# Kernel optimization log

Measured on AMD Instinct MI355X. Metric: run time of the kernel, lower is better.

Reference implementation:

```python
import jax, jax.numpy as jnp
import numpy as np

H = 16       # num_heads (groups for complex conv)
A = 32       # num frequency anchors
KSZ = 5      # complex conv kernel size
PAD = (KSZ - 1) // 2  # circular padding, matches ComplexConv1DLayer


def setup_inputs() -> dict:
    key = jax.random.key(0)
    ks = jax.random.split(key, 12)
    B, N, D = 4, 2048, 1024
    hid, ghid = 256, 256  # pooling MLP hidden, gate MLP hidden
    F = N // 2 + 1

    def rn(k, shp, s=0.02):
        return jax.random.normal(k, shp, jnp.float32) * s

    return {
        "x": jax.random.normal(ks[0], (B, N, D), jnp.float32),
        "Wv": rn(ks[1], (D, D)), "bv": jnp.zeros((D,), jnp.float32),
        "Wp1": rn(ks[2], (D, hid)), "bp1": jnp.zeros((hid,), jnp.float32),
        "Wp2": rn(ks[3], (hid, 1)), "bp2": jnp.zeros((1,), jnp.float32),
        "Wg1": rn(ks[4], (D, ghid)), "bg1": jnp.zeros((ghid,), jnp.float32),
        "Wg2": rn(ks[5], (ghid, 2 * H * A)), "bg2": jnp.zeros((2 * H * A,), jnp.float32),
        "mod_bias": jnp.zeros((F,), jnp.float32),
        "conv_kr": rn(ks[6], (KSZ,), 1.0 / np.sqrt(KSZ)),
        "conv_ki": rn(ks[7], (KSZ,), 1.0 / np.sqrt(KSZ)),
        "Wo": rn(ks[8], (D, D)), "bo": jnp.zeros((D,), jnp.float32),
    }


def reference(x, Wv, bv, Wp1, bp1, Wp2, bp2, Wg1, bg1, Wg2, bg2,
              mod_bias, conv_kr, conv_ki, Wo, bo):
    B, N, D = x.shape
    dh = D // H
    F = N // 2 + 1

    # value projection -> per-head sequences, rFFT over sequence axis
    v = (x @ Wv + bv).reshape(B, N, H, dh).transpose(0, 2, 1, 3)   # (B,H,N,dh)
    Vf = jnp.fft.rfft(v, axis=2)                                   # (B,H,F,dh) complex64

    # AttentionPoolingLayer: two-layer MLP scores -> softmax over seq -> weighted sum
    s = jax.nn.gelu(x @ Wp1 + bp1, approximate=False) @ Wp2 + bp2  # (B,N,1)
    w = jax.nn.softmax(s, axis=1)
    g = jnp.sum(x * w, axis=1)                                     # (B,D)

    # gate MLP -> complex anchors (B,H,A)
    a = (jax.nn.gelu(g @ Wg1 + bg1, approximate=False) @ Wg2 + bg2).reshape(B, H, A, 2)
    anch_r, anch_i = a[..., 0], a[..., 1]

    # ComplexInterpolationLayer: cubic interpolation of anchors to F bins
    gr = jax.image.resize(anch_r, (B, H, F), method="cubic")
    gi = jax.image.resize(anch_i, (B, H, F), method="cubic")
    gate = gr + 1j * gi                                            # (B,H,F)

    # ComplexModReLULayer: ReLU(|z|+b) * z / |z| with per-frequency bias
    mag = jnp.abs(gate)
    gate = gate * (jax.nn.relu(mag + mod_bias) / (mag + 1e-8))

    # ComplexConv1DLayer: circular-pad complex conv along frequency
    gp = jnp.concatenate([gate[..., -PAD:], gate, gate[..., :PAD]], axis=-1)
    ker = conv_kr.astype(jnp.complex64) + 1j * conv_ki.astype(jnp.complex64)
    gate = sum(ker[j] * gp[..., j:j + F] for j in range(KSZ))      # (B,H,F)

    # spectral gating + inverse FFT + output projection
    y = jnp.fft.irfft(Vf * gate[..., None], n=N, axis=2)           # (B,H,N,dh)
    y = y.transpose(0, 2, 1, 3).reshape(B, N, D)
    return y @ Wo + bo
```

## Files before the change

kernel.cpp:

```cpp
#include <hip/hip_runtime.h>
#include <math.h>

#define NSEQ 2048
#define DMOD 1024
#define NBATCH 4
#define NHEAD 16
#define NFREQ 1025

typedef unsigned short u16t;
typedef __attribute__((ext_vector_type(8))) short short8;
typedef __attribute__((ext_vector_type(4))) float f32x4;

__device__ __forceinline__ float gelu_exact(float x) {
  return 0.5f * x * (1.0f + erff(x * 0.70710678118654752440f));
}
__device__ __forceinline__ u16t bf16_rtn(float x) {
  unsigned u = __float_as_uint(x);
  return (u16t)((u + 0x7FFFu + ((u >> 16) & 1u)) >> 16);
}
__device__ __forceinline__ float bf16f(u16t h) {
  return __uint_as_float(((unsigned)h) << 16);
}
__device__ __forceinline__ void gload_lds16(const u16t* g, u16t* l) {
  __builtin_amdgcn_global_load_lds(
      (const __attribute__((address_space(1))) void*)g,
      (__attribute__((address_space(3))) void*)l, 16, 0, 0);
}

__global__ __launch_bounds__(256) void split_kernel(const float* __restrict__ in,
    u16t* __restrict__ hi, u16t* __restrict__ lo, int n8) {
  for (int i = blockIdx.x * blockDim.x + threadIdx.x; i < n8; i += gridDim.x * blockDim.x) {
    const float4* p = reinterpret_cast<const float4*>(in + (size_t)i * 8);
    float4 a = p[0], b = p[1];
    float vv[8] = {a.x, a.y, a.z, a.w, b.x, b.y, b.z, b.w};
    alignas(16) u16t th[8];
    alignas(16) u16t tl[8];
#pragma unroll
    for (int e = 0; e < 8; ++e) {
      u16t h = bf16_rtn(vv[e]);
      th[e] = h;
      tl[e] = bf16_rtn(vv[e] - bf16f(h));
    }
    *reinterpret_cast<uint4*>(hi + (size_t)i * 8) = *reinterpret_cast<const uint4*>(th);
    *reinterpret_cast<uint4*>(lo + (size_t)i * 8) = *reinterpret_cast<const uint4*>(tl);
  }
}

__global__ __launch_bounds__(256) void tsplit_kernel(const float* __restrict__ W,
    u16t* __restrict__ Th, u16t* __restrict__ Tl, int K, int N) {
  __shared__ float tile[32][33];
  int k0 = blockIdx.y * 32, n0 = blockIdx.x * 32;
  int r = threadIdx.x >> 5, c = threadIdx.x & 31;
#pragma unroll
  for (int i = 0; i < 4; ++i)
    tile[r + 8 * i][c] = W[(size_t)(k0 + r + 8 * i) * N + n0 + c];
  __syncthreads();
#pragma unroll
  for (int i = 0; i < 4; ++i) {
    int rr = r + 8 * i;
    float v = tile[c][rr];
    u16t h = bf16_rtn(v);
    Th[(size_t)(n0 + rr) * K + k0 + c] = h;
    Tl[(size_t)(n0 + rr) * K + k0 + c] = bf16_rtn(v - bf16f(h));
  }
}

__global__ __launch_bounds__(256) void tsplit2_kernel(
    const float* __restrict__ Wv, u16t* __restrict__ Tvh, u16t* __restrict__ Tvl,
    const float* __restrict__ Wp, u16t* __restrict__ Tph, u16t* __restrict__ Tpl) {
  __shared__ float tile[32][33];
  int bx = blockIdx.x;
  const float* W; u16t* Th; u16t* Tl; int N, n0;
  if (bx < 32) { W = Wv; Th = Tvh; Tl = Tvl; N = 1024; n0 = bx * 32; }
  else         { W = Wp; Th = Tph; Tl = Tpl; N = 256;  n0 = (bx - 32) * 32; }
  const int K = 1024;
  int k0 = blockIdx.y * 32;
  int r = threadIdx.x >> 5, c = threadIdx.x & 31;
#pragma unroll
  for (int i = 0; i < 4; ++i)
    tile[r + 8 * i][c] = W[(size_t)(k0 + r + 8 * i) * N + n0 + c];
  __syncthreads();
#pragma unroll
  for (int i = 0; i < 4; ++i) {
    int rr = r + 8 * i;
    float v = tile[c][rr];
    u16t h = bf16_rtn(v);
    Th[(size_t)(n0 + rr) * K + k0 + c] = h;
    Tl[(size_t)(n0 + rr) * K + k0 + c] = bf16_rtn(v - bf16f(h));
  }
}

__global__ __launch_bounds__(256) void gemm_fused_kernel(
    const u16t* __restrict__ Ah_g, const u16t* __restrict__ Al_g,
    const u16t* __restrict__ Bvh, const u16t* __restrict__ Bvl,
    const u16t* __restrict__ Bph, const u16t* __restrict__ Bpl,
    const float* __restrict__ bv, const float* __restrict__ bp1,
    const float* __restrict__ Wp2,
    float* __restrict__ vT, float* __restrict__ s_part) {
  __shared__ u16t Ahs[128 * 64], Als[128 * 64], Bhs[128 * 64], Bls[128 * 64];
  __shared__ u16t Php[32 * 64], Ppl[32 * 64];
  const int tid = threadIdx.x;
  const int lane = tid & 63, wave = tid >> 6;
  const int lr = lane & 15, lg = lane >> 4;
  const int wm0 = (wave >> 1) * 64, wn0 = (wave & 1) * 64;
  const int nwg = gridDim.x;
  const int L = (blockIdx.x & 7) * (nwg >> 3) + (blockIdx.x >> 3);
  const int m0 = (L >> 3) * 128;
  const int nblk = L & 7;
  const int n0 = nblk * 128;
  const int pc0 = nblk * 32;
  const int K = 1024;

  f32x4 acc[4][4];
#pragma unroll
  for (int i = 0; i < 4; ++i)
#pragma unroll
    for (int j = 0; j < 4; ++j) acc[i][j] = 0.0f;
  f32x4 accp[2][2];
#pragma unroll
  for (int i = 0; i < 2; ++i)
#pragma unroll
    for (int j = 0; j < 2; ++j) accp[i][j] = 0.0f;

  for (int k0 = 0; k0 < K; k0 += 64) {
#pragma unroll
    for (int q = 0; q < 4; ++q) {
      int cid = q * 256 + tid;
      int row = cid >> 3, grp = cid & 7;
      int koff = k0 + ((grp ^ (row & 7)) << 3);
      size_t ea = (size_t)(m0 + row) * K + koff;
      size_t eb = (size_t)(n0 + row) * K + koff;
      int lbase = q * 2048 + wave * 512;
      gload_lds16(Ah_g + ea, Ahs + lbase);
      gload_lds16(Al_g + ea, Als + lbase);
      gload_lds16(Bvh + eb, Bhs + lbase);
      gload_lds16(Bvl + eb, Bls + lbase);
    }
    {
      int row = tid >> 3, grp = tid & 7;
      int koff = k0 + ((grp ^ (row & 7)) << 3);
      size_t ep = (size_t)(pc0 + row) * K + koff;
      int lbase = wave * 512;
      gload_lds16(Bph + ep, Php + lbase);
      gload_lds16(Bpl + ep, Ppl + lbase);
    }
    __syncthreads();
#pragma unroll
    for (int kf = 0; kf < 2; ++kf) {
      short8 ah[4], al[4];
#pragma unroll
      for (int mi = 0; mi < 4; ++mi) {
        int r_ = wm0 + mi * 16 + lr;
        int g = (kf * 4 + lg) ^ (r_ & 7);
        ah[mi] = *reinterpret_cast<const short8*>(&Ahs[r_ * 64 + g * 8]);
        al[mi] = *reinterpret_cast<const short8*>(&Als[r_ * 64 + g * 8]);
      }
#pragma unroll
      for (int ni = 0; ni < 4; ++ni) {
        int r_ = wn0 + ni * 16 + lr;
        int g = (kf * 4 + lg) ^ (r_ & 7);
        short8 bh8 = *reinterpret_cast<const short8*>(&Bhs[r_ * 64 + g * 8]);
        short8 bl8 = *reinterpret_cast<const short8*>(&Bls[r_ * 64 + g * 8]);
#pragma unroll
        for (int mi = 0; mi < 4; ++mi) {
          acc[mi][ni] = __builtin_amdgcn_mfma_f32_16x16x32_bf16(ah[mi], bh8, acc[mi][ni], 0, 0, 0);
          acc[mi][ni] = __builtin_amdgcn_mfma_f32_16x16x32_bf16(ah[mi], bl8, acc[mi][ni], 0, 0, 0);
          acc[mi][ni] = __builtin_amdgcn_mfma_f32_16x16x32_bf16(al[mi], bh8, acc[mi][ni], 0, 0, 0);
        }
      }
      short8 pah[2], pal[2];
#pragma unroll
      for (int mi = 0; mi < 2; ++mi) {
        int r_ = wave * 32 + mi * 16 + lr;
        int g = (kf * 4 + lg) ^ (r_ & 7);
        pah[mi] = *reinterpret_cast<const short8*>(&Ahs[r_ * 64 + g * 8]);
        pal[mi] = *reinterpret_cast<const short8*>(&Als[r_ * 64 + g * 8]);
      }
#pragma unroll
      for (int ni = 0; ni < 2; ++ni) {
        int r_ = ni * 16 + lr;
        int g = (kf * 4 + lg) ^ (r_ & 7);
        short8 pbh = *reinterpret_cast<const short8*>(&Php[r_ * 64 + g * 8]);
        short8 pbl = *reinterpret_cast<const short8*>(&Ppl[r_ * 64 + g * 8]);
#pragma unroll
        for (int mi = 0; mi < 2; ++mi) {
          accp[mi][ni] = __builtin_amdgcn_mfma_f32_16x16x32_bf16(pah[mi], pbh, accp[mi][ni], 0, 0, 0);
          accp[mi][ni] = __builtin_amdgcn_mfma_f32_16x16x32_bf16(pah[mi], pbl, accp[mi][ni], 0, 0, 0);
          accp[mi][ni] = __builtin_amdgcn_mfma_f32_16x16x32_bf16(pal[mi], pbh, accp[mi][ni], 0, 0, 0);
        }
      }
    }
    __syncthreads();
  }
#pragma unroll
  for (int mi = 0; mi < 4; ++mi)
#pragma unroll
    for (int ni = 0; ni < 4; ++ni) {
      int col = n0 + wn0 + ni * 16 + lr;
      float bvv = bv[col];
      f32x4 a = acc[mi][ni];
      int mbase = m0 + wm0 + mi * 16 + lg * 4;
      int b = mbase >> 11, ss = mbase & 2047;
      float4 o4;
      o4.x = a[0] + bvv; o4.y = a[1] + bvv; o4.z = a[2] + bvv; o4.w = a[3] + bvv;
      *reinterpret_cast<float4*>(vT + (size_t)b * (DMOD * NSEQ) + (size_t)col * NSEQ + ss) = o4;
    }
  {
    float w2[2], bcol[2];
#pragma unroll
    for (int ni = 0; ni < 2; ++ni) {
      int col = pc0 + ni * 16 + lr;
      w2[ni] = Wp2[col];
      bcol[ni] = bp1[col];
    }
#pragma unroll
    for (int mi = 0; mi < 2; ++mi)
#pragma unroll
      for (int r = 0; r < 4; ++r) {
        float p = 0.f;
#pragma unroll
        for (int ni = 0; ni < 2; ++ni)
          p = fmaf(gelu_exact(accp[mi][ni][r] + bcol[ni]), w2[ni], p);
        p += __shfl_xor(p, 1);
        p += __shfl_xor(p, 2);
        p += __shfl_xor(p, 4);
        p += __shfl_xor(p, 8);
        if (lr == 0) {
          int row = m0 + wave * 32 + mi * 16 + lg * 4 + r;
          s_part[nblk * 8192 + row] = p;
        }
      }
  }
}

template<int NBLK>
__global__ __launch_bounds__(256) void mfma_gemm(
    const u16t* __restrict__ Ah_g, const u16t* __restrict__ Al_g,
    const u16t* __restrict__ Bh_g, const u16t* __restrict__ Bl_g,
    const float* __restrict__ bias,
    float* __restrict__ Cf,
    int N, int K) {
  __shared__ u16t Ahs[128 * 64], Als[128 * 64], Bhs[128 * 64], Bls[128 * 64];
  const int tid = threadIdx.x;
  const int lane = tid & 63, wave = tid >> 6;
  const int lr = lane & 15, lg = lane >> 4;
  const int wm0 = (wave >> 1) * 64, wn0 = (wave & 1) * 64;
  const int nwg = gridDim.x;
  const int L = (blockIdx.x & 7) * (nwg >> 3) + (blockIdx.x >> 3);
  const int m0 = (L / NBLK) * 128, n0 = (L % NBLK) * 128;

  f32x4 acc[4][4];
#pragma unroll
  for (int i = 0; i < 4; ++i)
#pragma unroll
    for (int j = 0; j < 4; ++j) acc[i][j] = 0.0f;

  for (int k0 = 0; k0 < K; k0 += 64) {
#pragma unroll
    for (int q = 0; q < 4; ++q) {
      int cid = q * 256 + tid;
      int row = cid >> 3, grp = cid & 7;
      int koff = k0 + ((grp ^ (row & 7)) << 3);
      size_t ea = (size_t)(m0 + row) * K + koff;
      size_t eb = (size_t)(n0 + row) * K + koff;
      int lbase = q * 2048 + wave * 512;
      gload_lds16(Ah_g + ea, Ahs + lbase);
      gload_lds16(Al_g + ea, Als + lbase);
      gload_lds16(Bh_g + eb, Bhs + lbase);
      gload_lds16(Bl_g + eb, Bls + lbase);
    }
    __syncthreads();
#pragma unroll
    for (int kf = 0; kf < 2; ++kf) {
      short8 ah[4], al[4];
#pragma unroll
      for (int mi = 0; mi < 4; ++mi) {
        int r_ = wm0 + mi * 16 + lr;
        int g = (kf * 4 + lg) ^ (r_ & 7);
        ah[mi] = *reinterpret_cast<const short8*>(&Ahs[r_ * 64 + g * 8]);
        al[mi] = *reinterpret_cast<const short8*>(&Als[r_ * 64 + g * 8]);
      }
#pragma unroll
      for (int ni = 0; ni < 4; ++ni) {
        int r_ = wn0 + ni * 16 + lr;
        int g = (kf * 4 + lg) ^ (r_ & 7);
        short8 bh8 = *reinterpret_cast<const short8*>(&Bhs[r_ * 64 + g * 8]);
        short8 bl8 = *reinterpret_cast<const short8*>(&Bls[r_ * 64 + g * 8]);
#pragma unroll
        for (int mi = 0; mi < 4; ++mi) {
          acc[mi][ni] = __builtin_amdgcn_mfma_f32_16x16x32_bf16(ah[mi], bh8, acc[mi][ni], 0, 0, 0);
          acc[mi][ni] = __builtin_amdgcn_mfma_f32_16x16x32_bf16(ah[mi], bl8, acc[mi][ni], 0, 0, 0);
          acc[mi][ni] = __builtin_amdgcn_mfma_f32_16x16x32_bf16(al[mi], bh8, acc[mi][ni], 0, 0, 0);
        }
      }
    }
    __syncthreads();
  }
#pragma unroll
  for (int mi = 0; mi < 4; ++mi)
#pragma unroll
    for (int ni = 0; ni < 4; ++ni) {
      int col = n0 + wn0 + ni * 16 + lr;
      float bvv = bias[col];
      f32x4 a = acc[mi][ni];
#pragma unroll
      for (int r = 0; r < 4; ++r) {
        int row = m0 + wm0 + mi * 16 + lg * 4 + r;
        Cf[(size_t)row * N + col] = a[r] + bvv;
      }
    }
}

#define PADI(i) ((i) + ((i) >> 5))

template<int HJ, int TWS>
__device__ __forceinline__ void fwd_reg_stage(float* vr, float* vi,
    const float* TWr, const float* TWi, int lane) {
  float twr_[HJ], twi_[HJ];
#pragma unroll
  for (int t = 0; t < HJ; ++t) {
    int m = (t * 64 + lane) * TWS;
    twr_[t] = TWr[PADI(m)]; twi_[t] = TWi[PADI(m)];
  }
#pragma unroll
  for (int j = 0; j < 16; ++j) {
    if (j & HJ) continue;
    int t = j & (HJ - 1);
    float ur = vr[j], ui = vi[j];
    float wr = vr[j + HJ], wi = vi[j + HJ];
    float dr = ur - wr, di = ui - wi;
    vr[j] = ur + wr; vi[j] = ui + wi;
    vr[j + HJ] = dr * twr_[t] - di * twi_[t];
    vi[j + HJ] = dr * twi_[t] + di * twr_[t];
  }
}

template<int S, int TWS>
__device__ __forceinline__ void fwd_lane_stage(float* vr, float* vi,
    const float* TWr, const float* TWi, int lane) {
  float twr_ = 1.0f, twi_ = 0.0f;
  if (S > 1) {
    int m = (lane & (S - 1)) * TWS;
    twr_ = TWr[PADI(m)]; twi_ = TWi[PADI(m)];
  }
  bool hi = (lane & S) != 0;
#pragma unroll
  for (int j = 0; j < 16; ++j) {
    float or_ = __shfl_xor(vr[j], S, 64);
    float oi_ = __shfl_xor(vi[j], S, 64);
    float sr = vr[j] + or_, si_ = vi[j] + oi_;
    float dr = or_ - vr[j], di = oi_ - vi[j];
    float rr = dr * twr_ - di * twi_;
    float ri = dr * twi_ + di * twr_;
    vr[j] = hi ? rr : sr;
    vi[j] = hi ? ri : si_;
  }
}

template<int S, int TWS>
__device__ __forceinline__ void inv_lane_stage(float* vr, float* vi,
    const float* TWr, const float* TWi, int lane) {
  float twr_ = 1.0f, twi_ = 0.0f;
  if (S > 1) {
    int m = (lane & (S - 1)) * TWS;
    twr_ = TWr[PADI(m)]; twi_ = -TWi[PADI(m)];
  }
  bool hi = (lane & S) != 0;
#pragma unroll
  for (int j = 0; j < 16; ++j) {
    float xr = vr[j], xi = vi[j];
    if (S > 1) {
      float pr = xr * twr_ - xi * twi_;
      float pi = xr * twi_ + xi * twr_;
      xr = hi ? pr : xr;
      xi = hi ? pi : xi;
    }
    float or_ = __shfl_xor(xr, S, 64);
    float oi_ = __shfl_xor(xi, S, 64);
    vr[j] = hi ? (or_ - xr) : (xr + or_);
    vi[j] = hi ? (oi_ - xi) : (xi + oi_);
  }
}

template<int HJ, int TWS>
__device__ __forceinline__ void inv_reg_stage(float* vr, float* vi,
    const float* TWr, const float* TWi, int lane) {
  float twr_[HJ], twi_[HJ];
#pragma unroll
  for (int t = 0; t < HJ; ++t) {
    int m = (t * 64 + lane) * TWS;
    twr_[t] = TWr[PADI(m)]; twi_[t] = -TWi[PADI(m)];
  }
#pragma unroll
  for (int j = 0; j < 16; ++j) {
    if (j & HJ) continue;
    int t = j & (HJ - 1);
    float ur = vr[j], ui = vi[j];
    float br = vr[j + HJ], bi = vi[j + HJ];
    float wr = br * twr_[t] - bi * twi_[t];
    float wi = br * twi_[t] + bi * twr_[t];
    vr[j] = ur + wr; vi[j] = ui + wi;
    vr[j + HJ] = ur - wr; vi[j + HJ] = ui - wi;
  }
}

__global__ __launch_bounds__(256) void conv_fft_kernel(
    float* __restrict__ vio, const float* __restrict__ gateb) {
  __shared__ float Zr[4][1056], Zi[4][1056];
  __shared__ float TWr[528], TWi[528];
  const int tid = threadIdx.x;
  const int lane = tid & 63, wave = tid >> 6;
  const int c0 = blockIdx.x * 4;
  const int b = blockIdx.y;
  const int bh = b * NHEAD + (c0 >> 6);
  const float* gate_bh = gateb + (size_t)bh * NFREQ * 2;

#pragma unroll
  for (int q = 0; q < 2; ++q) {
    int m = q * 256 + tid;
    float si, co;
    sincosf(-3.14159265358979323846f * (float)m * (1.0f / 512.0f), &si, &co);
    TWr[PADI(m)] = co; TWi[PADI(m)] = si;
  }
  __syncthreads();

  float* zr = Zr[wave];
  float* zi = Zi[wave];
  float* col = vio + ((size_t)b * DMOD + (c0 + wave)) * NSEQ;

  float vr[16], vi[16];
#pragma unroll
  for (int j = 0; j < 16; ++j) {
    float2 w2 = *reinterpret_cast<const float2*>(col + 2 * (j * 64 + lane));
    vr[j] = w2.x; vi[j] = w2.y;
  }

  fwd_reg_stage<8, 1>(vr, vi, TWr, TWi, lane);
  fwd_reg_stage<4, 2>(vr, vi, TWr, TWi, lane);
  fwd_reg_stage<2, 4>(vr, vi, TWr, TWi, lane);
  fwd_reg_stage<1, 8>(vr, vi, TWr, TWi, lane);
  fwd_lane_stage<32, 16>(vr, vi, TWr, TWi, lane);
  fwd_lane_stage<16, 32>(vr, vi, TWr, TWi, lane);
  fwd_lane_stage<8, 64>(vr, vi, TWr, TWi, lane);
  fwd_lane_stage<4, 128>(vr, vi, TWr, TWi, lane);
  fwd_lane_stage<2, 256>(vr, vi, TWr, TWi, lane);
  fwd_lane_stage<1, 0>(vr, vi, TWr, TWi, lane);

#pragma unroll
  for (int j = 0; j < 16; ++j) {
    int p = PADI(j * 64 + lane);
    zr[p] = vr[j]; zi[p] = vi[j];
  }
  asm volatile("s_waitcnt lgkmcnt(0)" ::: "memory");

  const float s1 = 1.0f / 1024.0f;
#pragma unroll
  for (int q = 0; q < 8; ++q) {
    int k = q * 64 + lane;
    if (k == 0) {
      float z0r = zr[0], z0i = zi[0];
      float X0 = z0r + z0i;
      float XN = z0r - z0i;
      float2 G0 = *reinterpret_cast<const float2*>(gate_bh + 0);
      float2 GN = *reinterpret_cast<const float2*>(gate_bh + 1024 * 2);
      float y0 = X0 * G0.x * s1;
      float yN = XN * GN.x * s1;
      zr[0] = 0.5f * (y0 + yN); zi[0] = 0.5f * (y0 - yN);
      float zmr = zr[1], zmi = zi[1];
      float X5r = zmr, X5i = -zmi;
      float2 G5 = *reinterpret_cast<const float2*>(gate_bh + 512 * 2);
      float Y5r = (X5r * G5.x - X5i * G5.y) * s1;
      float Y5i = (X5r * G5.y + X5i * G5.x) * s1;
      zr[1] = Y5r; zi[1] = -Y5i;
    } else {
      int kq = 1024 - k;
      int rp = PADI((int)(__brev((unsigned)k) >> 22));
      int rq = PADI((int)(__brev((unsigned)kq) >> 22));
      float Zkr = zr[rp], Zki = zi[rp];
      float Zqr = zr[rq], Zqi = zi[rq];
      float Er = 0.5f * (Zkr + Zqr), Ei = 0.5f * (Zki - Zqi);
      float Odr = 0.5f * (Zki + Zqi), Odi = -0.5f * (Zkr - Zqr);
      float ti, tr;
      sincosf(-3.14159265358979323846f * (float)k * (1.0f / 1024.0f), &ti, &tr);
      float Pr = Odr * tr - Odi * ti, Pi = Odr * ti + Odi * tr;
      float Xkr = Er + Pr, Xki = Ei + Pi;
      float Xqr = Er - Pr, Xqi = -(Ei - Pi);
      float2 Gk = *reinterpret_cast<const float2*>(gate_bh + k * 2);
      float2 Gq = *reinterpret_cast<const float2*>(gate_bh + kq * 2);
      float Ykr = (Xkr * Gk.x - Xki * Gk.y) * s1;
      float Yki = (Xkr * Gk.y + Xki * Gk.x) * s1;
      float Yqr = (Xqr * Gq.x - Xqi * Gq.y) * s1;
      float Yqi = (Xqr * Gq.y + Xqi * Gq.x) * s1;
      float E2r = 0.5f * (Ykr + Yqr), E2i = 0.5f * (Yki - Yqi);
      float D2r = 0.5f * (Ykr - Yqr), D2i = 0.5f * (Yki + Yqi);
      float O2r = D2r * tr + D2i * ti, O2i = D2i * tr - D2r * ti;
      zr[rp] = E2r - O2i; zi[rp] = E2i + O2r;
      zr[rq] = E2r + O2i; zi[rq] = O2r - E2i;
    }
  }
  asm volatile("s_waitcnt lgkmcnt(0)" ::: "memory");

#pragma unroll
  for (int j = 0; j < 16; ++j) {
    int p = PADI(j * 64 + lane);
    vr[j] = zr[p]; vi[j] = zi[p];
  }
  asm volatile("s_waitcnt lgkmcnt(0)" ::: "memory");

  inv_lane_stage<1, 0>(vr, vi, TWr, TWi, lane);
  inv_lane_stage<2, 256>(vr, vi, TWr, TWi, lane);
  inv_lane_stage<4, 128>(vr, vi, TWr, TWi, lane);
  inv_lane_stage<8, 64>(vr, vi, TWr, TWi, lane);
  inv_lane_stage<16, 32>(vr, vi, TWr, TWi, lane);
  inv_lane_stage<32, 16>(vr, vi, TWr, TWi, lane);
  inv_reg_stage<1, 8>(vr, vi, TWr, TWi, lane);
  inv_reg_stage<2, 4>(vr, vi, TWr, TWi, lane);
  inv_reg_stage<4, 2>(vr, vi, TWr, TWi, lane);
  inv_reg_stage<8, 1>(vr, vi, TWr, TWi, lane);

#pragma unroll
  for (int j = 0; j < 16; ++j) {
    *reinterpret_cast<float2*>(col + 2 * (j * 64 + lane)) = make_float2(vr[j], vi[j]);
  }
}

__global__ __launch_bounds__(256) void tysplit_kernel(
    const float* __restrict__ yT, u16t* __restrict__ yh, u16t* __restrict__ yl) {
  __shared__ float tile[64][65];
  int t0 = blockIdx.x * 64, c0 = blockIdx.y * 64, b = blockIdx.z;
  int r = threadIdx.x >> 4;
  int cc = (threadIdx.x & 15) * 4;
#pragma unroll
  for (int i = 0; i < 4; ++i) {
    int row = r + 16 * i;
    float4 w = *reinterpret_cast<const float4*>(
        yT + ((size_t)b * DMOD + c0 + row) * NSEQ + t0 + cc);
    tile[row][cc] = w.x; tile[row][cc + 1] = w.y;
    tile[row][cc + 2] = w.z; tile[row][cc + 3] = w.w;
  }
  __syncthreads();
#pragma unroll
  for (int i = 0; i < 4; ++i) {
    int tt = r + 16 * i;
    alignas(8) u16t hh[4], ll[4];
#pragma unroll
    for (int e = 0; e < 4; ++e) {
      float v = tile[cc + e][tt];
      u16t h = bf16_rtn(v);
      hh[e] = h;
      ll[e] = bf16_rtn(v - bf16f(h));
    }
    size_t o = ((size_t)b * NSEQ + t0 + tt) * DMOD + c0 + cc;
    *reinterpret_cast<ushort4*>(yh + o) = *reinterpret_cast<const ushort4*>(hh);
    *reinterpret_cast<ushort4*>(yl + o) = *reinterpret_cast<const ushort4*>(ll);
  }
}

__global__ __launch_bounds__(256) void pool_partial_kernel(
    const float* __restrict__ x, const float* __restrict__ s_part,
    const float* __restrict__ bp2, float* __restrict__ gpart) {
  int chunk = blockIdx.x, b = blockIdx.y;
  int tid = threadIdx.x;
  __shared__ float red[256];
  __shared__ float wsh[128];
  float bp = bp2[0];
  float sv[8];
  float m = -1e30f;
#pragma unroll
  for (int q = 0; q < 8; ++q) {
    int row = b * NSEQ + q * 256 + tid;
    float v = bp;
#pragma unroll
    for (int c = 0; c < 8; ++c) v += s_part[c * 8192 + row];
    sv[q] = v;
    m = fmaxf(m, v);
  }
  red[tid] = m; __syncthreads();
  for (int o = 128; o; o >>= 1) { if (tid < o) red[tid] = fmaxf(red[tid], red[tid + o]); __syncthreads(); }
  float bm = red[0]; __syncthreads();
  float sum = 0.f;
#pragma unroll
  for (int q = 0; q < 8; ++q) sum += expf(sv[q] - bm);
  red[tid] = sum; __syncthreads();
  for (int o = 128; o; o >>= 1) { if (tid < o) red[tid] += red[tid + o]; __syncthreads(); }
  float inv = 1.0f / red[0];
  __syncthreads();
  int n0 = chunk * 128;
  if (tid < 128) {
    int row = b * NSEQ + n0 + tid;
    float v = bp;
#pragma unroll
    for (int c = 0; c < 8; ++c) v += s_part[c * 8192 + row];
    wsh[tid] = expf(v - bm) * inv;
  }
  __syncthreads();
  float acc[4] = {};
  for (int n = 0; n < 128; ++n) {
    float wn = wsh[n];
    const float* xr = &x[((size_t)b * NSEQ + n0 + n) * DMOD];
#pragma unroll
    for (int q = 0; q < 4; ++q) acc[q] = fmaf(wn, xr[tid + 256 * q], acc[q]);
  }
  float* gp = &gpart[((size_t)b * 16 + chunk) * DMOD];
#pragma unroll
  for (int q = 0; q < 4; ++q) gp[tid + 256 * q] = acc[q];
}

__global__ __launch_bounds__(256) void pool_reduce_mlp1_kernel(
    const float* __restrict__ gpart, const float* __restrict__ Wg1,
    float* __restrict__ part1) {
  int kb = blockIdx.x, b = blockIdx.y;
  int tid = threadIdx.x;
  int k0 = kb * 64;
  __shared__ float g_s[64];
  if (tid < 64) {
    float acc = 0.f;
#pragma unroll
    for (int j = 0; j < 16; ++j)
      acc += gpart[((size_t)b * 16 + j) * DMOD + k0 + tid];
    g_s[tid] = acc;
  }
  __syncthreads();
  float acc = 0.f;
#pragma unroll 8
  for (int i = 0; i < 64; ++i)
    acc = fmaf(g_s[i], Wg1[(size_t)(k0 + i) * 256 + tid], acc);
  part1[((size_t)b * 16 + kb) * 256 + tid] = acc;
}

__device__ __forceinline__ float keys_cubic(float x) {
  if (x >= 2.0f) return 0.0f;
  if (x >= 1.0f) return ((-0.5f * x + 2.5f) * x - 4.0f) * x + 2.0f;
  return ((1.5f * x - 2.5f) * x) * x + 1.0f;
}

__global__ __launch_bounds__(256) void gate_kernel(
    const float* __restrict__ part1, const float* __restrict__ bg1,
    const float* __restrict__ Wg2, const float* __restrict__ bg2,
    const float* __restrict__ mod_bias,
    const float* __restrict__ kr5, const float* __restrict__ ki5,
    float* __restrict__ gate_out) {
  int bh = blockIdx.x;
  int tid = threadIdx.x;
  __shared__ float hs_s[256];
  __shared__ float anch_s[64];
  __shared__ float ar_[32], ai_[32];
  __shared__ float gr[NFREQ], gi[NFREQ];
  int b = bh >> 4, h = bh & 15;
  {
    float a1 = bg1[tid];
#pragma unroll
    for (int j = 0; j < 16; ++j)
      a1 += part1[((size_t)b * 16 + j) * 256 + tid];
    hs_s[tid] = gelu_exact(a1);
  }
  __syncthreads();
  if (tid < 64) {
    int cc = h * 64 + tid;
    float a2 = bg2[cc];
    for (int i = 0; i < 256; ++i) a2 = fmaf(hs_s[i], Wg2[(size_t)i * 1024 + cc], a2);
    anch_s[tid] = a2;
  }
  __syncthreads();
  if (tid < 32) {
    ar_[tid] = anch_s[tid * 2 + 0];
    ai_[tid] = anch_s[tid * 2 + 1];
  }
  __syncthreads();
  const float inv_scale = 32.0f / 1025.0f;
  for (int f = tid; f < NFREQ; f += 256) {
    float c = (f + 0.5f) * inv_scale - 0.5f;
    int j0 = (int)floorf(c) - 1;
    float wr = 0.f, wi = 0.f, wsum = 0.f;
#pragma unroll
    for (int u = 0; u < 4; ++u) {
      int j = j0 + u;
      if (j < 0 || j > 31) continue;
      float w = keys_cubic(fabsf(c - (float)j));
      wsum += w;
      wr = fmaf(w, ar_[j], wr);
      wi = fmaf(w, ai_[j], wi);
    }
    float invw = 1.0f / wsum;
    wr *= invw; wi *= invw;
    float mag = sqrtf(wr * wr + wi * wi);
    float scale = fmaxf(mag + mod_bias[f], 0.0f) / (mag + 1e-8f);
    gr[f] = wr * scale;
    gi[f] = wi * scale;
  }
  __syncthreads();
  float k_r[5], k_i[5];
#pragma unroll
  for (int j = 0; j < 5; ++j) { k_r[j] = kr5[j]; k_i[j] = ki5[j]; }
  for (int f = tid; f < NFREQ; f += 256) {
    float cr = 0.f, ci = 0.f;
#pragma unroll
    for (int j = 0; j < 5; ++j) {
      int idx = f + j - 2;
      if (idx < 0) idx += NFREQ;
      else if (idx >= NFREQ) idx -= NFREQ;
      float a = gr[idx], bb = gi[idx];
      cr = fmaf(k_r[j], a, cr); cr = fmaf(-k_i[j], bb, cr);
      ci = fmaf(k_r[j], bb, ci); ci = fmaf(k_i[j], a, ci);
    }
    gate_out[((size_t)bh * NFREQ + f) * 2 + 0] = cr;
    gate_out[((size_t)bh * NFREQ + f) * 2 + 1] = ci;
  }
}

extern "C" void kernel_launch(void* const* d_in, const int* in_sizes, int n_in,
                              void* d_out, int out_size, void* d_ws, size_t ws_size,
                              hipStream_t stream) {
  const float* x        = (const float*)d_in[0];
  const float* Wv       = (const float*)d_in[1];
  const float* bv       = (const float*)d_in[2];
  const float* Wp1      = (const float*)d_in[3];
  const float* bp1      = (const float*)d_in[4];
  const float* Wp2      = (const float*)d_in[5];
  const float* bp2      = (const float*)d_in[6];
  const float* Wg1      = (const float*)d_in[7];
  const float* bg1      = (const float*)d_in[8];
  const float* Wg2      = (const float*)d_in[9];
  const float* bg2      = (const float*)d_in[10];
  const float* mod_bias = (const float*)d_in[11];
  const float* ckr      = (const float*)d_in[12];
  const float* cki      = (const float*)d_in[13];
  const float* Wo       = (const float*)d_in[14];
  const float* bo       = (const float*)d_in[15];

  const int M = NBATCH * NSEQ;
  const size_t MD = (size_t)M * DMOD;
  char* wsb = (char*)d_ws;

  u16t* x_hi = (u16t*)wsb;
  u16t* x_lo = x_hi + MD;
  u16t* y_hi = x_hi;
  u16t* y_lo = x_lo;
  u16t* WT_h = (u16t*)(wsb + (size_t)32 * 1024 * 1024);
  u16t* WT_l = (u16t*)(wsb + (size_t)34 * 1024 * 1024);
  u16t* WTp1_h = (u16t*)(wsb + (size_t)36 * 1024 * 1024);
  u16t* WTp1_l = (u16t*)(wsb + (size_t)36 * 1024 * 1024 + 524288);
  float* s_part = (float*)(wsb + (size_t)37 * 1024 * 1024);
  float* gpart = (float*)(wsb + (size_t)36 * 1024 * 1024);
  float* part1 = gpart + 65536;
  float* gateb = part1 + 4096;

  float* vT  = (float*)d_out;
  float* out = (float*)d_out;

  dim3 blk(256);

  split_kernel<<<dim3(2048), blk, 0, stream>>>(x, x_hi, x_lo, (int)(MD / 8));
  tsplit2_kernel<<<dim3(40, 32), blk, 0, stream>>>(Wv, WT_h, WT_l, Wp1, WTp1_h, WTp1_l);
  gemm_fused_kernel<<<dim3(512), blk, 0, stream>>>(
      x_hi, x_lo, WT_h, WT_l, WTp1_h, WTp1_l, bv, bp1, Wp2, vT, s_part);
  tsplit_kernel<<<dim3(1024 / 32, 1024 / 32), blk, 0, stream>>>(Wo, WT_h, WT_l, 1024, 1024);
  pool_partial_kernel<<<dim3(16, NBATCH), blk, 0, stream>>>(x, s_part, bp2, gpart);
  pool_reduce_mlp1_kernel<<<dim3(16, NBATCH), blk, 0, stream>>>(gpart, Wg1, part1);
  gate_kernel<<<dim3(NBATCH * NHEAD), blk, 0, stream>>>(
      part1, bg1, Wg2, bg2, mod_bias, ckr, cki, gateb);
  conv_fft_kernel<<<dim3(DMOD / 4, NBATCH), blk, 0, stream>>>(vT, gateb);
  tysplit_kernel<<<dim3(NSEQ / 64, DMOD / 64, NBATCH), blk, 0, stream>>>(vT, y_hi, y_lo);
  mfma_gemm<8><<<dim3((DMOD / 128) * (M / 128)), blk, 0, stream>>>(
      y_hi, y_lo, WT_h, WT_l, bo, out, DMOD, 1024);
}
```

Before: 204.0 us.

## Fuse prep kernels, fold y transpose-split into FFT, merge pooling stages

Merges the x split and the weight transpose-splits into one launch, and merges the Wo transpose-split with the pooling partial kernel. It folds the pool reduction and first gate-MLP layer into the gate kernel. The FFT kernel now processes 16 columns per 1024-thread block and writes the bf16 hi/lo split of y directly through LDS. This removes the separate tysplit pass and its fp32 write and re-read of vT. The cost is a larger block with heavy LDS use (about 135KB) and lower occupancy for the FFT, plus a serial 1024-long Wg1 dot product per thread in the gate kernel.

```diff
diff --git a/kernel.cpp b/kernel.cpp
--- a/kernel.cpp
+++ b/kernel.cpp
@@ -27,66 +27,50 @@
       (__attribute__((address_space(3))) void*)l, 16, 0, 0);
 }
 
-__global__ __launch_bounds__(256) void split_kernel(const float* __restrict__ in,
-    u16t* __restrict__ hi, u16t* __restrict__ lo, int n8) {
-  for (int i = blockIdx.x * blockDim.x + threadIdx.x; i < n8; i += gridDim.x * blockDim.x) {
-    const float4* p = reinterpret_cast<const float4*>(in + (size_t)i * 8);
-    float4 a = p[0], b = p[1];
-    float vv[8] = {a.x, a.y, a.z, a.w, b.x, b.y, b.z, b.w};
-    alignas(16) u16t th[8];
-    alignas(16) u16t tl[8];
-#pragma unroll
-    for (int e = 0; e < 8; ++e) {
-      u16t h = bf16_rtn(vv[e]);
-      th[e] = h;
-      tl[e] = bf16_rtn(vv[e] - bf16f(h));
-    }
-    *reinterpret_cast<uint4*>(hi + (size_t)i * 8) = *reinterpret_cast<const uint4*>(th);
-    *reinterpret_cast<uint4*>(lo + (size_t)i * 8) = *reinterpret_cast<const uint4*>(tl);
-  }
-}
-
-__global__ __launch_bounds__(256) void tsplit_kernel(const float* __restrict__ W,
-    u16t* __restrict__ Th, u16t* __restrict__ Tl, int K, int N) {
-  __shared__ float tile[32][33];
-  int k0 = blockIdx.y * 32, n0 = blockIdx.x * 32;
-  int r = threadIdx.x >> 5, c = threadIdx.x & 31;
-#pragma unroll
-  for (int i = 0; i < 4; ++i)
-    tile[r + 8 * i][c] = W[(size_t)(k0 + r + 8 * i) * N + n0 + c];
-  __syncthreads();
-#pragma unroll
-  for (int i = 0; i < 4; ++i) {
-    int rr = r + 8 * i;
-    float v = tile[c][rr];
-    u16t h = bf16_rtn(v);
-    Th[(size_t)(n0 + rr) * K + k0 + c] = h;
-    Tl[(size_t)(n0 + rr) * K + k0 + c] = bf16_rtn(v - bf16f(h));
-  }
-}
-
-__global__ __launch_bounds__(256) void tsplit2_kernel(
+__global__ __launch_bounds__(256) void prep_kernel(
+    const float* __restrict__ x, u16t* __restrict__ x_hi, u16t* __restrict__ x_lo,
     const float* __restrict__ Wv, u16t* __restrict__ Tvh, u16t* __restrict__ Tvl,
-    const float* __restrict__ Wp, u16t* __restrict__ Tph, u16t* __restrict__ Tpl) {
+    const float* __restrict__ Wp1, u16t* __restrict__ Tph, u16t* __restrict__ Tpl) {
   __shared__ float tile[32][33];
   int bx = blockIdx.x;
-  const float* W; u16t* Th; u16t* Tl; int N, n0;
-  if (bx < 32) { W = Wv; Th = Tvh; Tl = Tvl; N = 1024; n0 = bx * 32; }
-  else         { W = Wp; Th = Tph; Tl = Tpl; N = 256;  n0 = (bx - 32) * 32; }
-  const int K = 1024;
-  int k0 = blockIdx.y * 32;
-  int r = threadIdx.x >> 5, c = threadIdx.x & 31;
-#pragma unroll
-  for (int i = 0; i < 4; ++i)
-    tile[r + 8 * i][c] = W[(size_t)(k0 + r + 8 * i) * N + n0 + c];
-  __syncthreads();
-#pragma unroll
-  for (int i = 0; i < 4; ++i) {
-    int rr = r + 8 * i;
-    float v = tile[c][rr];
-    u16t h = bf16_rtn(v);
-    Th[(size_t)(n0 + rr) * K + k0 + c] = h;
-    Tl[(size_t)(n0 + rr) * K + k0 + c] = bf16_rtn(v - bf16f(h));
+  int tid = threadIdx.x;
+  if (bx < 2048) {
+    const int n8 = (NBATCH * NSEQ * DMOD) / 8;
+    for (int i = bx * 256 + tid; i < n8; i += 2048 * 256) {
+      const float4* p = reinterpret_cast<const float4*>(x + (size_t)i * 8);
+      float4 a = p[0], b = p[1];
+      float vv[8] = {a.x, a.y, a.z, a.w, b.x, b.y, b.z, b.w};
+      alignas(16) u16t th[8];
+      alignas(16) u16t tl[8];
+#pragma unroll
+      for (int e = 0; e < 8; ++e) {
+        u16t h = bf16_rtn(vv[e]);
+        th[e] = h;
+        tl[e] = bf16_rtn(vv[e] - bf16f(h));
+      }
+      *reinterpret_cast<uint4*>(x_hi + (size_t)i * 8) = *reinterpret_cast<const uint4*>(th);
+      *reinterpret_cast<uint4*>(x_lo + (size_t)i * 8) = *reinterpret_cast<const uint4*>(tl);
+    }
+  } else {
+    int idx = bx - 2048;
+    int wcol = idx % 40, k0 = (idx / 40) * 32;
+    const float* W; u16t* Th; u16t* Tl; int N, n0;
+    if (wcol < 32) { W = Wv;  Th = Tvh; Tl = Tvl; N = 1024; n0 = wcol * 32; }
+    else           { W = Wp1; Th = Tph; Tl = Tpl; N = 256;  n0 = (wcol - 32) * 32; }
+    const int K = 1024;
+    int r = tid >> 5, c = tid & 31;
+#pragma unroll
+    for (int i = 0; i < 4; ++i)
+      tile[r + 8 * i][c] = W[(size_t)(k0 + r + 8 * i) * N + n0 + c];
+    __syncthreads();
+#pragma unroll
+    for (int i = 0; i < 4; ++i) {
+      int rr = r + 8 * i;
+      float v = tile[c][rr];
+      u16t h = bf16_rtn(v);
+      Th[(size_t)(n0 + rr) * K + k0 + c] = h;
+      Tl[(size_t)(n0 + rr) * K + k0 + c] = bf16_rtn(v - bf16f(h));
+    }
   }
 }
 
@@ -312,6 +296,7 @@
 }
 
 #define PADI(i) ((i) + ((i) >> 5))
+#define ZSTRIDE 1057
 
 template<int HJ, int TWS>
 __device__ __forceinline__ void fwd_reg_stage(float* vr, float* vi,
@@ -404,29 +389,28 @@
   }
 }
 
-__global__ __launch_bounds__(256) void conv_fft_kernel(
-    float* __restrict__ vio, const float* __restrict__ gateb) {
-  __shared__ float Zr[4][1056], Zi[4][1056];
+__global__ __launch_bounds__(1024) void conv_fft_kernel(
+    const float* __restrict__ vT, const float* __restrict__ gateb,
+    u16t* __restrict__ yh, u16t* __restrict__ yl) {
+  __shared__ float Zr[16 * ZSTRIDE], Zi[16 * ZSTRIDE];
   __shared__ float TWr[528], TWi[528];
   const int tid = threadIdx.x;
   const int lane = tid & 63, wave = tid >> 6;
-  const int c0 = blockIdx.x * 4;
+  const int c0 = blockIdx.x * 16;
   const int b = blockIdx.y;
   const int bh = b * NHEAD + (c0 >> 6);
   const float* gate_bh = gateb + (size_t)bh * NFREQ * 2;
 
-#pragma unroll
-  for (int q = 0; q < 2; ++q) {
-    int m = q * 256 + tid;
+  if (tid < 512) {
     float si, co;
-    sincosf(-3.14159265358979323846f * (float)m * (1.0f / 512.0f), &si, &co);
-    TWr[PADI(m)] = co; TWi[PADI(m)] = si;
+    sincosf(-3.14159265358979323846f * (float)tid * (1.0f / 512.0f), &si, &co);
+    TWr[PADI(tid)] = co; TWi[PADI(tid)] = si;
   }
   __syncthreads();
 
-  float* zr = Zr[wave];
-  float* zi = Zi[wave];
-  float* col = vio + ((size_t)b * DMOD + (c0 + wave)) * NSEQ;
+  float* zr = Zr + wave * ZSTRIDE;
+  float* zi = Zi + wave * ZSTRIDE;
+  const float* col = vT + ((size_t)b * DMOD + (c0 + wave)) * NSEQ;
 
   float vr[16], vi[16];
 #pragma unroll
@@ -520,112 +504,105 @@
 
 #pragma unroll
   for (int j = 0; j < 16; ++j) {
-    *reinterpret_cast<float2*>(col + 2 * (j * 64 + lane)) = make_float2(vr[j], vi[j]);
-  }
-}
-
-__global__ __launch_bounds__(256) void tysplit_kernel(
-    const float* __restrict__ yT, u16t* __restrict__ yh, u16t* __restrict__ yl) {
-  __shared__ float tile[64][65];
-  int t0 = blockIdx.x * 64, c0 = blockIdx.y * 64, b = blockIdx.z;
-  int r = threadIdx.x >> 4;
-  int cc = (threadIdx.x & 15) * 4;
-#pragma unroll
-  for (int i = 0; i < 4; ++i) {
-    int row = r + 16 * i;
-    float4 w = *reinterpret_cast<const float4*>(
-        yT + ((size_t)b * DMOD + c0 + row) * NSEQ + t0 + cc);
-    tile[row][cc] = w.x; tile[row][cc + 1] = w.y;
-    tile[row][cc + 2] = w.z; tile[row][cc + 3] = w.w;
+    int p = PADI(j * 64 + lane);
+    zr[p] = vr[j]; zi[p] = vi[j];
   }
   __syncthreads();
-#pragma unroll
-  for (int i = 0; i < 4; ++i) {
-    int tt = r + 16 * i;
-    alignas(8) u16t hh[4], ll[4];
-#pragma unroll
-    for (int e = 0; e < 4; ++e) {
-      float v = tile[cc + e][tt];
-      u16t h = bf16_rtn(v);
-      hh[e] = h;
-      ll[e] = bf16_rtn(v - bf16f(h));
-    }
-    size_t o = ((size_t)b * NSEQ + t0 + tt) * DMOD + c0 + cc;
-    *reinterpret_cast<ushort4*>(yh + o) = *reinterpret_cast<const ushort4*>(hh);
-    *reinterpret_cast<ushort4*>(yl + o) = *reinterpret_cast<const ushort4*>(ll);
-  }
-}
-
-__global__ __launch_bounds__(256) void pool_partial_kernel(
+
+  {
+    alignas(16) u16t he[16], le[16], ho[16], lo_[16];
+    int p = PADI(tid);
+#pragma unroll
+    for (int w = 0; w < 16; ++w) {
+      float re = Zr[w * ZSTRIDE + p];
+      float im = Zi[w * ZSTRIDE + p];
+      u16t hr = bf16_rtn(re);
+      he[w] = hr; le[w] = bf16_rtn(re - bf16f(hr));
+      u16t hm = bf16_rtn(im);
+      ho[w] = hm; lo_[w] = bf16_rtn(im - bf16f(hm));
+    }
+    size_t o0 = ((size_t)b * NSEQ + 2 * tid) * DMOD + c0;
+    size_t o1 = o0 + DMOD;
+    *reinterpret_cast<uint4*>(yh + o0) = reinterpret_cast<const uint4*>(he)[0];
+    *reinterpret_cast<uint4*>(yh + o0 + 8) = reinterpret_cast<const uint4*>(he)[1];
+    *reinterpret_cast<uint4*>(yl + o0) = reinterpret_cast<const uint4*>(le)[0];
+    *reinterpret_cast<uint4*>(yl + o0 + 8) = reinterpret_cast<const uint4*>(le)[1];
+    *reinterpret_cast<uint4*>(yh + o1) = reinterpret_cast<const uint4*>(ho)[0];
+    *reinterpret_cast<uint4*>(yh + o1 + 8) = reinterpret_cast<const uint4*>(ho)[1];
+    *reinterpret_cast<uint4*>(yl + o1) = reinterpret_cast<const uint4*>(lo_)[0];
+    *reinterpret_cast<uint4*>(yl + o1 + 8) = reinterpret_cast<const uint4*>(lo_)[1];
+  }
+}
+
+__global__ __launch_bounds__(256) void wo_pool_kernel(
+    const float* __restrict__ Wo, u16t* __restrict__ Toh, u16t* __restrict__ Tol,
     const float* __restrict__ x, const float* __restrict__ s_part,
     const float* __restrict__ bp2, float* __restrict__ gpart) {
-  int chunk = blockIdx.x, b = blockIdx.y;
-  int tid = threadIdx.x;
+  __shared__ float tile[32][33];
   __shared__ float red[256];
   __shared__ float wsh[128];
-  float bp = bp2[0];
-  float sv[8];
-  float m = -1e30f;
-#pragma unroll
-  for (int q = 0; q < 8; ++q) {
-    int row = b * NSEQ + q * 256 + tid;
-    float v = bp;
-#pragma unroll
-    for (int c = 0; c < 8; ++c) v += s_part[c * 8192 + row];
-    sv[q] = v;
-    m = fmaxf(m, v);
-  }
-  red[tid] = m; __syncthreads();
-  for (int o = 128; o; o >>= 1) { if (tid < o) red[tid] = fmaxf(red[tid], red[tid + o]); __syncthreads(); }
-  float bm = red[0]; __syncthreads();
-  float sum = 0.f;
-#pragma unroll
-  for (int q = 0; q < 8; ++q) sum += expf(sv[q] - bm);
-  red[tid] = sum; __syncthreads();
-  for (int o = 128; o; o >>= 1) { if (tid < o) red[tid] += red[tid + o]; __syncthreads(); }
-  float inv = 1.0f / red[0];
-  __syncthreads();
-  int n0 = chunk * 128;
-  if (tid < 128) {
-    int row = b * NSEQ + n0 + tid;
-    float v = bp;
-#pragma unroll
-    for (int c = 0; c < 8; ++c) v += s_part[c * 8192 + row];
-    wsh[tid] = expf(v - bm) * inv;
-  }
-  __syncthreads();
-  float acc[4] = {};
-  for (int n = 0; n < 128; ++n) {
-    float wn = wsh[n];
-    const float* xr = &x[((size_t)b * NSEQ + n0 + n) * DMOD];
-#pragma unroll
-    for (int q = 0; q < 4; ++q) acc[q] = fmaf(wn, xr[tid + 256 * q], acc[q]);
-  }
-  float* gp = &gpart[((size_t)b * 16 + chunk) * DMOD];
-#pragma unroll
-  for (int q = 0; q < 4; ++q) gp[tid + 256 * q] = acc[q];
-}
-
-__global__ __launch_bounds__(256) void pool_reduce_mlp1_kernel(
-    const float* __restrict__ gpart, const float* __restrict__ Wg1,
-    float* __restrict__ part1) {
-  int kb = blockIdx.x, b = blockIdx.y;
+  int bx = blockIdx.x;
   int tid = threadIdx.x;
-  int k0 = kb * 64;
-  __shared__ float g_s[64];
-  if (tid < 64) {
-    float acc = 0.f;
-#pragma unroll
-    for (int j = 0; j < 16; ++j)
-      acc += gpart[((size_t)b * 16 + j) * DMOD + k0 + tid];
-    g_s[tid] = acc;
-  }
-  __syncthreads();
-  float acc = 0.f;
-#pragma unroll 8
-  for (int i = 0; i < 64; ++i)
-    acc = fmaf(g_s[i], Wg1[(size_t)(k0 + i) * 256 + tid], acc);
-  part1[((size_t)b * 16 + kb) * 256 + tid] = acc;
+  if (bx < 1024) {
+    int n0 = (bx & 31) * 32, k0 = (bx >> 5) * 32;
+    int r = tid >> 5, c = tid & 31;
+#pragma unroll
+    for (int i = 0; i < 4; ++i)
+      tile[r + 8 * i][c] = Wo[(size_t)(k0 + r + 8 * i) * 1024 + n0 + c];
+    __syncthreads();
+#pragma unroll
+    for (int i = 0; i < 4; ++i) {
+      int rr = r + 8 * i;
+      float v = tile[c][rr];
+      u16t h = bf16_rtn(v);
+      Toh[(size_t)(n0 + rr) * 1024 + k0 + c] = h;
+      Tol[(size_t)(n0 + rr) * 1024 + k0 + c] = bf16_rtn(v - bf16f(h));
+    }
+  } else {
+    int idx = bx - 1024;
+    int chunk = idx & 15, b = idx >> 4;
+    float bp = bp2[0];
+    float sv[8];
+    float m = -1e30f;
+#pragma unroll
+    for (int q = 0; q < 8; ++q) {
+      int row = b * NSEQ + q * 256 + tid;
+      float v = bp;
+#pragma unroll
+      for (int c = 0; c < 8; ++c) v += s_part[c * 8192 + row];
+      sv[q] = v;
+      m = fmaxf(m, v);
+    }
+    red[tid] = m; __syncthreads();
+    for (int o = 128; o; o >>= 1) { if (tid < o) red[tid] = fmaxf(red[tid], red[tid + o]); __syncthreads(); }
+    float bm = red[0]; __syncthreads();
+    float sum = 0.f;
+#pragma unroll
+    for (int q = 0; q < 8; ++q) sum += expf(sv[q] - bm);
+    red[tid] = sum; __syncthreads();
+    for (int o = 128; o; o >>= 1) { if (tid < o) red[tid] += red[tid + o]; __syncthreads(); }
+    float inv = 1.0f / red[0];
+    __syncthreads();
+    int n0 = chunk * 128;
+    if (tid < 128) {
+      int row = b * NSEQ + n0 + tid;
+      float v = bp;
+#pragma unroll
+      for (int c = 0; c < 8; ++c) v += s_part[c * 8192 + row];
+      wsh[tid] = expf(v - bm) * inv;
+    }
+    __syncthreads();
+    float acc[4] = {};
+    for (int n = 0; n < 128; ++n) {
+      float wn = wsh[n];
+      const float* xr = &x[((size_t)b * NSEQ + n0 + n) * DMOD];
+#pragma unroll
+      for (int q = 0; q < 4; ++q) acc[q] = fmaf(wn, xr[tid + 256 * q], acc[q]);
+    }
+    float* gp = &gpart[((size_t)b * 16 + chunk) * DMOD];
+#pragma unroll
+    for (int q = 0; q < 4; ++q) gp[tid + 256 * q] = acc[q];
+  }
 }
 
 __device__ __forceinline__ float keys_cubic(float x) {
@@ -635,24 +612,37 @@
 }
 
 __global__ __launch_bounds__(256) void gate_kernel(
-    const float* __restrict__ part1, const float* __restrict__ bg1,
+    const float* __restrict__ gpart, const float* __restrict__ Wg1,
+    const float* __restrict__ bg1,
     const float* __restrict__ Wg2, const float* __restrict__ bg2,
     const float* __restrict__ mod_bias,
     const float* __restrict__ kr5, const float* __restrict__ ki5,
     float* __restrict__ gate_out) {
   int bh = blockIdx.x;
   int tid = threadIdx.x;
+  __shared__ float g_s[1024];
   __shared__ float hs_s[256];
   __shared__ float anch_s[64];
   __shared__ float ar_[32], ai_[32];
   __shared__ float gr[NFREQ], gi[NFREQ];
   int b = bh >> 4, h = bh & 15;
+  for (int d = tid; d < 1024; d += 256) {
+    float acc = 0.f;
+#pragma unroll
+    for (int j = 0; j < 16; ++j)
+      acc += gpart[((size_t)b * 16 + j) * DMOD + d];
+    g_s[d] = acc;
+  }
+  __syncthreads();
   {
-    float a1 = bg1[tid];
-#pragma unroll
-    for (int j = 0; j < 16; ++j)
-      a1 += part1[((size_t)b * 16 + j) * 256 + tid];
-    hs_s[tid] = gelu_exact(a1);
+    float a0 = 0.f, a1 = 0.f, a2 = 0.f, a3 = 0.f;
+    for (int i = 0; i < 1024; i += 4) {
+      a0 = fmaf(g_s[i], Wg1[(size_t)i * 256 + tid], a0);
+      a1 = fmaf(g_s[i + 1], Wg1[(size_t)(i + 1) * 256 + tid], a1);
+      a2 = fmaf(g_s[i + 2], Wg1[(size_t)(i + 2) * 256 + tid], a2);
+      a3 = fmaf(g_s[i + 3], Wg1[(size_t)(i + 3) * 256 + tid], a3);
+    }
+    hs_s[tid] = gelu_exact(bg1[tid] + ((a0 + a1) + (a2 + a3)));
   }
   __syncthreads();
   if (tid < 64) {
@@ -742,25 +732,23 @@
   u16t* WTp1_l = (u16t*)(wsb + (size_t)36 * 1024 * 1024 + 524288);
   float* s_part = (float*)(wsb + (size_t)37 * 1024 * 1024);
   float* gpart = (float*)(wsb + (size_t)36 * 1024 * 1024);
-  float* part1 = gpart + 65536;
-  float* gateb = part1 + 4096;
+  float* gateb = gpart + 65536;
 
   float* vT  = (float*)d_out;
   float* out = (float*)d_out;
 
   dim3 blk(256);
 
-  split_kernel<<<dim3(2048), blk, 0, stream>>>(x, x_hi, x_lo, (int)(MD / 8));
-  tsplit2_kernel<<<dim3(40, 32), blk, 0, stream>>>(Wv, WT_h, WT_l, Wp1, WTp1_h, WTp1_l);
+  prep_kernel<<<dim3(2048 + 1280), blk, 0, stream>>>(
+      x, x_hi, x_lo, Wv, WT_h, WT_l, Wp1, WTp1_h, WTp1_l);
   gemm_fused_kernel<<<dim3(512), blk, 0, stream>>>(
       x_hi, x_lo, WT_h, WT_l, WTp1_h, WTp1_l, bv, bp1, Wp2, vT, s_part);
-  tsplit_kernel<<<dim3(1024 / 32, 1024 / 32), blk, 0, stream>>>(Wo, WT_h, WT_l, 1024, 1024);
-  pool_partial_kernel<<<dim3(16, NBATCH), blk, 0, stream>>>(x, s_part, bp2, gpart);
-  pool_reduce_mlp1_kernel<<<dim3(16, NBATCH), blk, 0, stream>>>(gpart, Wg1, part1);
+  wo_pool_kernel<<<dim3(1024 + 64), blk, 0, stream>>>(
+      Wo, WT_h, WT_l, x, s_part, bp2, gpart);
   gate_kernel<<<dim3(NBATCH * NHEAD), blk, 0, stream>>>(
-      part1, bg1, Wg2, bg2, mod_bias, ckr, cki, gateb);
-  conv_fft_kernel<<<dim3(DMOD / 4, NBATCH), blk, 0, stream>>>(vT, gateb);
-  tysplit_kernel<<<dim3(NSEQ / 64, DMOD / 64, NBATCH), blk, 0, stream>>>(vT, y_hi, y_lo);
+      gpart, Wg1, bg1, Wg2, bg2, mod_bias, ckr, cki, gateb);
+  conv_fft_kernel<<<dim3(DMOD / 16, NBATCH), dim3(1024), 0, stream>>>(
+      vT, gateb, y_hi, y_lo);
   mfma_gemm<8><<<dim3((DMOD / 128) * (M / 128)), blk, 0, stream>>>(
       y_hi, y_lo, WT_h, WT_l, bo, out, DMOD, 1024);
 }
```

Result: slower. 231.5 us (+13.5%).

## Fuse bf16 split transpose into FFT kernel via shared-memory staging

Applied to the files above, without the earlier changes.

The FFT conv kernel now processes 16 columns per 1024-thread block and, instead of writing the fp32 result back to global memory, stages it in LDS and directly emits the transposed bf16 hi/lo split outputs. This removes the separate tysplit kernel along with its extra global read and write of the full fp32 activation. In exchange, the block uses much more LDS (about 135KB) and 1024 threads, which lowers occupancy, and the output stores are 32-byte chunks strided by the row length.

```diff
diff --git a/kernel.cpp b/kernel.cpp
--- a/kernel.cpp
+++ b/kernel.cpp
@@ -312,6 +312,7 @@
 }
 
 #define PADI(i) ((i) + ((i) >> 5))
+#define ZSTRIDE 1057
 
 template<int HJ, int TWS>
 __device__ __forceinline__ void fwd_reg_stage(float* vr, float* vi,
@@ -404,29 +405,28 @@
   }
 }
 
-__global__ __launch_bounds__(256) void conv_fft_kernel(
-    float* __restrict__ vio, const float* __restrict__ gateb) {
-  __shared__ float Zr[4][1056], Zi[4][1056];
+__global__ __launch_bounds__(1024) void conv_fft_kernel(
+    const float* __restrict__ vT, const float* __restrict__ gateb,
+    u16t* __restrict__ yh, u16t* __restrict__ yl) {
+  __shared__ float Zr[16 * ZSTRIDE], Zi[16 * ZSTRIDE];
   __shared__ float TWr[528], TWi[528];
   const int tid = threadIdx.x;
   const int lane = tid & 63, wave = tid >> 6;
-  const int c0 = blockIdx.x * 4;
+  const int c0 = blockIdx.x * 16;
   const int b = blockIdx.y;
   const int bh = b * NHEAD + (c0 >> 6);
   const float* gate_bh = gateb + (size_t)bh * NFREQ * 2;
 
-#pragma unroll
-  for (int q = 0; q < 2; ++q) {
-    int m = q * 256 + tid;
+  if (tid < 512) {
     float si, co;
-    sincosf(-3.14159265358979323846f * (float)m * (1.0f / 512.0f), &si, &co);
-    TWr[PADI(m)] = co; TWi[PADI(m)] = si;
-  }
-  __syncthreads();
-
-  float* zr = Zr[wave];
-  float* zi = Zi[wave];
-  float* col = vio + ((size_t)b * DMOD + (c0 + wave)) * NSEQ;
+    sincosf(-3.14159265358979323846f * (float)tid * (1.0f / 512.0f), &si, &co);
+    TWr[PADI(tid)] = co; TWi[PADI(tid)] = si;
+  }
+  __syncthreads();
+
+  float* zr = Zr + wave * ZSTRIDE;
+  float* zi = Zi + wave * ZSTRIDE;
+  const float* col = vT + ((size_t)b * DMOD + (c0 + wave)) * NSEQ;
 
   float vr[16], vi[16];
 #pragma unroll
@@ -520,39 +520,33 @@
 
 #pragma unroll
   for (int j = 0; j < 16; ++j) {
-    *reinterpret_cast<float2*>(col + 2 * (j * 64 + lane)) = make_float2(vr[j], vi[j]);
-  }
-}
-
-__global__ __launch_bounds__(256) void tysplit_kernel(
-    const float* __restrict__ yT, u16t* __restrict__ yh, u16t* __restrict__ yl) {
-  __shared__ float tile[64][65];
-  int t0 = blockIdx.x * 64, c0 = blockIdx.y * 64, b = blockIdx.z;
-  int r = threadIdx.x >> 4;
-  int cc = (threadIdx.x & 15) * 4;
-#pragma unroll
-  for (int i = 0; i < 4; ++i) {
-    int row = r + 16 * i;
-    float4 w = *reinterpret_cast<const float4*>(
-        yT + ((size_t)b * DMOD + c0 + row) * NSEQ + t0 + cc);
-    tile[row][cc] = w.x; tile[row][cc + 1] = w.y;
-    tile[row][cc + 2] = w.z; tile[row][cc + 3] = w.w;
-  }
-  __syncthreads();
-#pragma unroll
-  for (int i = 0; i < 4; ++i) {
-    int tt = r + 16 * i;
-    alignas(8) u16t hh[4], ll[4];
-#pragma unroll
-    for (int e = 0; e < 4; ++e) {
-      float v = tile[cc + e][tt];
-      u16t h = bf16_rtn(v);
-      hh[e] = h;
-      ll[e] = bf16_rtn(v - bf16f(h));
-    }
-    size_t o = ((size_t)b * NSEQ + t0 + tt) * DMOD + c0 + cc;
-    *reinterpret_cast<ushort4*>(yh + o) = *reinterpret_cast<const ushort4*>(hh);
-    *reinterpret_cast<ushort4*>(yl + o) = *reinterpret_cast<const ushort4*>(ll);
+    int p = PADI(j * 64 + lane);
+    zr[p] = vr[j]; zi[p] = vi[j];
+  }
+  __syncthreads();
+
+  {
+    alignas(16) u16t he[16], le[16], ho[16], lo_[16];
+    int p = PADI(tid);
+#pragma unroll
+    for (int w = 0; w < 16; ++w) {
+      float re = Zr[w * ZSTRIDE + p];
+      float im = Zi[w * ZSTRIDE + p];
+      u16t hr = bf16_rtn(re);
+      he[w] = hr; le[w] = bf16_rtn(re - bf16f(hr));
+      u16t hm = bf16_rtn(im);
+      ho[w] = hm; lo_[w] = bf16_rtn(im - bf16f(hm));
+    }
+    size_t o0 = ((size_t)b * NSEQ + 2 * tid) * DMOD + c0;
+    size_t o1 = o0 + DMOD;
+    *reinterpret_cast<uint4*>(yh + o0) = reinterpret_cast<const uint4*>(he)[0];
+    *reinterpret_cast<uint4*>(yh + o0 + 8) = reinterpret_cast<const uint4*>(he)[1];
+    *reinterpret_cast<uint4*>(yl + o0) = reinterpret_cast<const uint4*>(le)[0];
+    *reinterpret_cast<uint4*>(yl + o0 + 8) = reinterpret_cast<const uint4*>(le)[1];
+    *reinterpret_cast<uint4*>(yh + o1) = reinterpret_cast<const uint4*>(ho)[0];
+    *reinterpret_cast<uint4*>(yh + o1 + 8) = reinterpret_cast<const uint4*>(ho)[1];
+    *reinterpret_cast<uint4*>(yl + o1) = reinterpret_cast<const uint4*>(lo_)[0];
+    *reinterpret_cast<uint4*>(yl + o1 + 8) = reinterpret_cast<const uint4*>(lo_)[1];
   }
 }
 
@@ -759,8 +753,8 @@
   pool_reduce_mlp1_kernel<<<dim3(16, NBATCH), blk, 0, stream>>>(gpart, Wg1, part1);
   gate_kernel<<<dim3(NBATCH * NHEAD), blk, 0, stream>>>(
       part1, bg1, Wg2, bg2, mod_bias, ckr, cki, gateb);
-  conv_fft_kernel<<<dim3(DMOD / 4, NBATCH), blk, 0, stream>>>(vT, gateb);
-  tysplit_kernel<<<dim3(NSEQ / 64, DMOD / 64, NBATCH), blk, 0, stream>>>(vT, y_hi, y_lo);
+  conv_fft_kernel<<<dim3(DMOD / 16, NBATCH), dim3(1024), 0, stream>>>(
+      vT, gateb, y_hi, y_lo);
   mfma_gemm<8><<<dim3((DMOD / 128) * (M / 128)), blk, 0, stream>>>(
       y_hi, y_lo, WT_h, WT_l, bo, out, DMOD, 1024);
 }
```

Result: faster. 199.9 us (-2.0%).
